# Performance work log

Hardware: AMD Instinct MI355X
Metric: run time of the kernel (lower is better)

## Reference

```python
import jax, jax.numpy as jnp
import numpy as np

B, S, D, N = 8, 4096, 1024, 64
EPS = 1e-5


def setup_inputs() -> dict:
    key = jax.random.key(0)
    ks = jax.random.split(key, 6)
    sD = 1.0 / np.sqrt(D)
    sN = 1.0 / np.sqrt(N)
    return {
        "x": jax.random.normal(ks[0], (B, S, D), dtype=jnp.float32),
        "ln_w": jnp.ones((D,), jnp.float32),
        "ln_b": jnp.zeros((D,), jnp.float32),
        "Wi": jax.random.normal(ks[1], (N, D), jnp.float32) * sD,
        "bi": jnp.zeros((N,), jnp.float32),
        "Wf": jax.random.normal(ks[2], (N, D), jnp.float32) * sD,
        "bf": jnp.zeros((N,), jnp.float32),
        "Wz": jax.random.normal(ks[3], (N, D), jnp.float32) * sD,
        "bz": jnp.zeros((N,), jnp.float32),
        "Wo": jax.random.normal(ks[4], (N, D), jnp.float32) * sD,
        "bo": jnp.zeros((N,), jnp.float32),
        "Wp": jax.random.normal(ks[5], (D, N), jnp.float32) * sN,
        "bp": jnp.zeros((D,), jnp.float32),
    }


def reference(x, ln_w, ln_b, Wi, bi, Wf, bf, Wz, bz, Wo, bo, Wp, bp):
    # LayerNorm over last dim (eps matches torch default 1e-5)
    mu = jnp.mean(x, axis=-1, keepdims=True)
    var = jnp.mean(jnp.square(x - mu), axis=-1, keepdims=True)
    xn = (x - mu) * jax.lax.rsqrt(var + EPS) * ln_w + ln_b

    # Precompute all four projections as batched GEMMs: (B,S,N)
    log_i = jnp.clip(jnp.einsum('bsd,nd->bsn', xn, Wi) + bi, -20.0, 20.0)
    log_f = jnp.clip(jnp.einsum('bsd,nd->bsn', xn, Wf) + bf, -20.0, 20.0)
    z = jnp.tanh(jnp.einsum('bsd,nd->bsn', xn, Wz) + bz)
    o = jax.nn.sigmoid(jnp.einsum('bsd,nd->bsn', xn, Wo) + bo)

    # Stabilized exponential-gated recurrence via lax.scan over time
    def step(carry, inp):
        c, m = carry
        li, lf, zt, ot = inp
        m_new = jnp.maximum(m + lf, li)
        i_s = jnp.exp(li - m_new)
        f_s = jnp.exp(m + lf - m_new)
        c = f_s * c + i_s * zt
        h = ot * jnp.tanh(c)
        return (c, m_new), h

    c0 = jnp.zeros((x.shape[0], log_i.shape[-1]), x.dtype)
    m0 = jnp.zeros_like(c0)
    # time-major inputs: (S,B,N)
    tm = lambda a: jnp.swapaxes(a, 0, 1)
    _, h_seq = jax.lax.scan(step, (c0, m0), (tm(log_i), tm(log_f), tm(z), tm(o)))
    h_seq = jnp.swapaxes(h_seq, 0, 1)  # (B,S,N)

    return jnp.einsum('bsn,dn->bsd', h_seq, Wp) + bp
```

## Files before the change

### kernel.cpp

```cpp
#include <hip/hip_runtime.h>
#include <hip/hip_bf16.h>

#define BB 8
#define SS 4096
#define DD 1024
#define NN 64
#define ROWS (BB * SS)
#define GLD 256
#define NCHUNK 256
#define CLEN 16
#define GSTRIDE 194

typedef _Float16 f16;
using f16x8 = __attribute__((ext_vector_type(8))) _Float16;
using f32x4 = __attribute__((ext_vector_type(4))) float;

__global__ __launch_bounds__(256) void prep_all(const float* __restrict__ Wi, const float* __restrict__ bi,
                                                const float* __restrict__ Wf, const float* __restrict__ bfv,
                                                const float* __restrict__ Wz, const float* __restrict__ bz,
                                                const float* __restrict__ Wo, const float* __restrict__ bo,
                                                const float* __restrict__ Wp,
                                                const float* __restrict__ ln_w, const float* __restrict__ ln_b,
                                                f16* __restrict__ Wpk, f16* __restrict__ Wpf,
                                                float* __restrict__ ball, float* __restrict__ e_all) {
    if (blockIdx.x < 384) {
        int i = blockIdx.x * 256 + threadIdx.x;
        if (i < 32768) {
            int l = i & 63, cb = (i >> 6) & 15, s = i >> 10;
            int r = cb * 16 + (l & 15);
            int c = s * 32 + (l >> 4) * 8;
            int g = r >> 6, rem = r & 63;
            const float* W = (g == 0) ? Wi : (g == 1) ? Wf : (g == 2) ? Wz : Wo;
            const float* src = W + rem * 1024 + c;
            const float* lwp = ln_w + c;
            f16x8 v;
            #pragma unroll
            for (int e = 0; e < 8; ++e) v[e] = (f16)(src[e] * lwp[e]);
            *reinterpret_cast<f16x8*>(Wpk + (size_t)s * 8192 + cb * 512 + l * 8) = v;
        } else if (i < 32768 + 65536) {
            int j = i - 32768;
            Wpf[j] = (f16)Wp[j];
        }
    } else {
        int j = (blockIdx.x - 384) * 4 + (threadIdx.x >> 6);
        int lane = threadIdx.x & 63;
        int g = j >> 6, rem = j & 63;
        const float* W  = (g == 0) ? Wi : (g == 1) ? Wf : (g == 2) ? Wz : Wo;
        const float* bs = (g == 0) ? bi : (g == 1) ? bfv : (g == 2) ? bz : bo;
        const float* row = W + rem * 1024;
        float d = 0.0f, e = 0.0f;
        #pragma unroll
        for (int t = 0; t < 16; ++t) {
            int k = lane + 64 * t;
            float w = row[k];
            e += ln_w[k] * w;
            d += ln_b[k] * w;
        }
        #pragma unroll
        for (int off = 1; off < 64; off <<= 1) {
            e += __shfl_xor(e, off);
            d += __shfl_xor(d, off);
        }
        if (lane == 0) { ball[j] = bs[rem] + d; e_all[j] = e; }
    }
}

__global__ __launch_bounds__(512, 1) void gate_gemm(const float* __restrict__ x,
                                                    const f16* __restrict__ Wpk,
                                                    const float* __restrict__ ball,
                                                    const float* __restrict__ e_all,
                                                    float* __restrict__ gates,
                                                    float4* __restrict__ s4) {
    int bm = blockIdx.x * 128;
    int tid = threadIdx.x;
    int wid = tid >> 6, lane = tid & 63;
    int wm = wid >> 2, wn = wid & 3;
    int lrow = lane & 15, lkg = lane >> 4;
    int srow = tid >> 2, skg = tid & 3;

    __shared__ __align__(16) f16 Wlds[2][16384];
    __shared__ __align__(16) f16 Xlds[2][8192];
    __shared__ float2 stats_lds[128];

    const float4* xrow = reinterpret_cast<const float4*>(x + (size_t)(bm + srow) * DD) + skg * 4;
    float4 A0, A1, A2, A3, B0, B1, B2, B3;
    uint4 W0, W1, W2, W3;
    const uint4* wsrc = reinterpret_cast<const uint4*>(Wpk) + wid * 256 + lane;

    auto loadA = [&](int s) { const float4* p = xrow + s * 16; A0 = p[0]; A1 = p[1]; A2 = p[2]; A3 = p[3]; };
    auto loadB = [&](int s) { const float4* p = xrow + s * 16; B0 = p[0]; B1 = p[1]; B2 = p[2]; B3 = p[3]; };
    auto loadW = [&](int s) { const uint4* p = wsrc + (size_t)s * 2048; W0 = p[0]; W1 = p[64]; W2 = p[128]; W3 = p[192]; };
    auto writeW = [&](int buf) {
        uint4* d = reinterpret_cast<uint4*>((char*)&Wlds[buf][0] + wid * 4096) + lane;
        d[0] = W0; d[64] = W1; d[128] = W2; d[192] = W3;
    };

    float s1 = 0.0f, s2 = 0.0f;
    auto writeXv = [&](float4 v0, float4 v1, float4 v2, float4 v3, int buf) {
        float xv[16] = {v0.x, v0.y, v0.z, v0.w, v1.x, v1.y, v1.z, v1.w,
                        v2.x, v2.y, v2.z, v2.w, v3.x, v3.y, v3.z, v3.w};
        f16x8 p0, p1;
        #pragma unroll
        for (int e = 0; e < 8; ++e) {
            s1 += xv[e] + xv[8 + e];
            s2 += xv[e] * xv[e] + xv[8 + e] * xv[8 + e];
            p0[e] = (f16)xv[e];
            p1[e] = (f16)xv[8 + e];
        }
        char* base = (char*)&Xlds[buf][0] + srow * 128;
        int r7 = srow & 7;
        *reinterpret_cast<f16x8*>(base + 16 * ((2 * skg) ^ r7))     = p0;
        *reinterpret_cast<f16x8*>(base + 16 * ((2 * skg + 1) ^ r7)) = p1;
    };

    f32x4 acc[4][4] = {};
    auto compute = [&](int buf) {
        #pragma unroll
        for (int h = 0; h < 2; ++h) {
            f16x8 a[4];
            #pragma unroll
            for (int mf = 0; mf < 4; ++mf) {
                int row = wm * 64 + mf * 16 + lrow;
                a[mf] = *reinterpret_cast<const f16x8*>(
                    (const char*)&Xlds[buf][0] + row * 128 + 16 * ((4 * h + lkg) ^ (row & 7)));
            }
            #pragma unroll
            for (int nf = 0; nf < 4; ++nf) {
                int cb = wn * 4 + nf;
                f16x8 w = *reinterpret_cast<const f16x8*>(
                    (const char*)&Wlds[buf][0] + h * 16384 + cb * 1024 + lane * 16);
                #pragma unroll
                for (int mf = 0; mf < 4; ++mf)
                    acc[mf][nf] = __builtin_amdgcn_mfma_f32_16x16x32_f16(a[mf], w, acc[mf][nf], 0, 0, 0);
            }
        }
    };
    auto stepSync = [&]() {
        asm volatile("s_waitcnt lgkmcnt(0)" ::: "memory");
        __builtin_amdgcn_s_barrier();
        __builtin_amdgcn_sched_barrier(0);
    };

    loadA(0); loadB(1); loadW(0);
    writeW(0);
    writeXv(A0, A1, A2, A3, 0);
    loadA(2); loadW(1);
    stepSync();

    for (int it = 0; it < 8; ++it) {
        int s = 2 * it;
        compute(0);
        writeW(1);
        writeXv(B0, B1, B2, B3, 1);
        if (s + 2 <= 15) loadW(s + 2);
        if (s + 3 <= 15) loadB(s + 3);
        stepSync();
        compute(1);
        if (s + 2 <= 15) {
            writeW(0);
            writeXv(A0, A1, A2, A3, 0);
        }
        if (s + 3 <= 15) loadW(s + 3);
        if (s + 4 <= 15) loadA(s + 4);
        stepSync();
    }

    s1 += __shfl_xor(s1, 1); s2 += __shfl_xor(s2, 1);
    s1 += __shfl_xor(s1, 2); s2 += __shfl_xor(s2, 2);
    if ((tid & 3) == 0) {
        float mu = s1 * (1.0f / DD);
        float var = s2 * (1.0f / DD) - mu * mu;
        float rsd = rsqrtf(var + 1e-5f);
        float2 st; st.x = mu * rsd; st.y = rsd;
        stats_lds[srow] = st;
    }
    __syncthreads();

    float* glds = reinterpret_cast<float*>(&Wlds[0][0]);
    int c0 = wn * 64;
    int rb = (lane >> 4) * 4;
    #pragma unroll
    for (int mf = 0; mf < 4; ++mf) {
        #pragma unroll
        for (int nf = 0; nf < 4; ++nf) {
            int col = c0 + nf * 16 + (lane & 15);
            float bc = ball[col];
            float ec = e_all[col];
            #pragma unroll
            for (int r = 0; r < 4; ++r) {
                int rl = wm * 64 + mf * 16 + rb + r;
                float2 st = stats_lds[rl];
                float v = acc[mf][nf][r] * st.y + bc - st.x * ec;
                float res;
                if (wn == 0 || wn == 1)      res = fminf(fmaxf(v, -20.0f), 20.0f);
                else if (wn == 2)            res = tanhf(v);
                else                         res = 1.0f / (1.0f + expf(-v));
                gates[(size_t)(bm + rl) * GLD + col] = res;
                if (wm == 0 && wn < 3)
                    glds[(mf * 16 + rb + r) * GSTRIDE + col] = res;
            }
        }
    }
    __syncthreads();

    int b = bm >> 12;
    int cb0 = (bm & 4095) >> 4;
    auto scanChunk = [&]() {
        int lr0 = (wid & 3) * 16;
        float Lf = 0.0f, m = -1e30f, c = 0.0f;
        #pragma unroll
        for (int j = 0; j < 16; ++j) {
            const float* g = glds + (lr0 + j) * GSTRIDE;
            float li = g[lane], lf = g[64 + lane], z = g[128 + lane];
            Lf += lf;
            float ma = m + lf;
            float mn = fmaxf(ma, li);
            c = __expf(ma - mn) * c + __expf(li - mn) * z;
            m = mn;
        }
        float4 v; v.x = Lf; v.y = m; v.z = c; v.w = 0.0f;
        s4[(size_t)(b * NCHUNK + cb0 + wid) * 64 + lane] = v;
    };

    if (wm == 0) scanChunk();
    __syncthreads();

    if (wm == 1 && wn < 3) {
        #pragma unroll
        for (int mf = 0; mf < 4; ++mf) {
            #pragma unroll
            for (int nf = 0; nf < 4; ++nf) {
                int col = c0 + nf * 16 + (lane & 15);
                float bc = ball[col];
                float ec = e_all[col];
                #pragma unroll
                for (int r = 0; r < 4; ++r) {
                    int rl = 64 + mf * 16 + rb + r;
                    float2 st = stats_lds[rl];
                    float v = acc[mf][nf][r] * st.y + bc - st.x * ec;
                    float res;
                    if (wn == 0 || wn == 1)      res = fminf(fmaxf(v, -20.0f), 20.0f);
                    else                         res = tanhf(v);
                    glds[(mf * 16 + rb + r) * GSTRIDE + col] = res;
                }
            }
        }
    }
    __syncthreads();
    if (wm == 1) scanChunk();
}

__global__ __launch_bounds__(64) void scan_b(const float4* __restrict__ s4,
                                             float2* __restrict__ c2) {
    int b = blockIdx.x;
    int n = threadIdx.x;
    size_t base = (size_t)b * NCHUNK * 64 + n;
    float c = 0.0f, m = 0.0f;
    float4 cur[16];
    #pragma unroll
    for (int d = 0; d < 16; ++d) cur[d] = s4[base + (size_t)d * 64];
    for (int kb = 0; kb < NCHUNK; kb += 16) {
        float4 nxt[16];
        if (kb + 16 < NCHUNK) {
            #pragma unroll
            for (int d = 0; d < 16; ++d) nxt[d] = s4[base + (size_t)(kb + 16 + d) * 64];
        }
        #pragma unroll
        for (int d = 0; d < 16; ++d) {
            float2 ci; ci.x = m; ci.y = c;
            c2[base + (size_t)(kb + d) * 64] = ci;
            float4 v = cur[d];
            float ma = m + v.x;
            float mo = fmaxf(ma, v.y);
            c = expf(ma - mo) * c + expf(v.y - mo) * v.z;
            m = mo;
        }
        #pragma unroll
        for (int d = 0; d < 16; ++d) cur[d] = nxt[d];
    }
}

__global__ __launch_bounds__(256) void scan_c(const float* __restrict__ gates,
                                              const float2* __restrict__ c2,
                                              f16* __restrict__ h) {
    int w = blockIdx.x * 4 + (threadIdx.x >> 6);
    int lane = threadIdx.x & 63;
    int b = w >> 8, k = w & (NCHUNK - 1);
    int t0 = k * CLEN;
    float2 ci = c2[(size_t)(b * NCHUNK + k) * 64 + lane];
    float m = ci.x, c = ci.y;
    const float* gp = gates + ((size_t)(b * SS + t0)) * GLD + lane;
    f16* hp = h + ((size_t)(b * SS + t0)) * NN + lane;
    for (int t = 0; t < CLEN; ++t) {
        float li = gp[0], lf = gp[64], z = gp[128], o = gp[192];
        gp += GLD;
        float ma = m + lf;
        float mn = fmaxf(ma, li);
        c = expf(ma - mn) * c + expf(li - mn) * z;
        m = mn;
        *hp = (f16)(o * tanhf(c));
        hp += NN;
    }
}

__global__ __launch_bounds__(256) void out_gemm(const f16* __restrict__ h,
                                                const f16* __restrict__ Wpf,
                                                const float* __restrict__ bp,
                                                float* __restrict__ out) {
    int tid = threadIdx.x, wid = tid >> 6, lane = tid & 63;
    int r0 = (blockIdx.x >> 1) * 32;
    int c0 = (blockIdx.x & 1) * 512 + wid * 128;
    int lrow = lane & 15, lk = (lane >> 4) * 8;

    f32x4 acc[2][8] = {};
    #pragma unroll
    for (int ks = 0; ks < 2; ++ks) {
        int kk = ks * 32;
        f16x8 a[2], bfr[8];
        #pragma unroll
        for (int mf = 0; mf < 2; ++mf)
            a[mf] = *reinterpret_cast<const f16x8*>(h + (size_t)(r0 + mf * 16 + lrow) * NN + kk + lk);
        #pragma unroll
        for (int nf = 0; nf < 8; ++nf)
            bfr[nf] = *reinterpret_cast<const f16x8*>(Wpf + (size_t)(c0 + nf * 16 + lrow) * NN + kk + lk);
        #pragma unroll
        for (int mf = 0; mf < 2; ++mf)
            #pragma unroll
            for (int nf = 0; nf < 8; ++nf)
                acc[mf][nf] = __builtin_amdgcn_mfma_f32_16x16x32_f16(a[mf], bfr[nf], acc[mf][nf], 0, 0, 0);
    }
    int rb = (lane >> 4) * 4;
    #pragma unroll
    for (int nf = 0; nf < 8; ++nf) {
        int col = c0 + nf * 16 + (lane & 15);
        float bias = bp[col];
        #pragma unroll
        for (int mf = 0; mf < 2; ++mf) {
            #pragma unroll
            for (int r = 0; r < 4; ++r) {
                int row = r0 + mf * 16 + rb + r;
                out[(size_t)row * DD + col] = acc[mf][nf][r] + bias;
            }
        }
    }
}

extern "C" void kernel_launch(void* const* d_in, const int* in_sizes, int n_in,
                              void* d_out, int out_size, void* d_ws, size_t ws_size,
                              hipStream_t stream) {
    const float* x    = (const float*)d_in[0];
    const float* ln_w = (const float*)d_in[1];
    const float* ln_b = (const float*)d_in[2];
    const float* Wi   = (const float*)d_in[3];
    const float* bi   = (const float*)d_in[4];
    const float* Wf   = (const float*)d_in[5];
    const float* bfv  = (const float*)d_in[6];
    const float* Wz   = (const float*)d_in[7];
    const float* bz   = (const float*)d_in[8];
    const float* Wo   = (const float*)d_in[9];
    const float* bo   = (const float*)d_in[10];
    const float* Wp   = (const float*)d_in[11];
    const float* bp   = (const float*)d_in[12];
    float* out = (float*)d_out;

    float* gates = (float*)d_out;
    float4* s4 = (float4*)((float*)d_out + 9 * 1024 * 1024);
    float2* c2 = (float2*)((float*)d_out + 10 * 1024 * 1024);

    char* w = (char*)d_ws;
    f16* h    = (f16*)w; w += (size_t)ROWS * NN * 2;
    f16* Wpk  = (f16*)w; w += 32 * 8192 * 2;
    f16* Wpf  = (f16*)w; w += 1024 * 64 * 2;
    float* ball   = (float*)w;    w += 256 * 4;
    float* e_all  = (float*)w;    w += 256 * 4;

    prep_all<<<448, 256, 0, stream>>>(Wi, bi, Wf, bfv, Wz, bz, Wo, bo, Wp,
                                      ln_w, ln_b, Wpk, Wpf, ball, e_all);
    gate_gemm<<<ROWS / 128, 512, 0, stream>>>(x, Wpk, ball, e_all, gates, s4);
    scan_b<<<BB, 64, 0, stream>>>(s4, c2);
    scan_c<<<(BB * NCHUNK) / 4, 256, 0, stream>>>(gates, c2, h);
    out_gemm<<<(ROWS / 32) * 2, 256, 0, stream>>>(h, Wpf, bp, out);
}
```

Baseline: 135.9 us.

## Fuse chunk rescan into output GEMM and single-pass gate chunk scan

Merges the per-chunk recurrence replay (scan_c) into the output projection kernel, so h is built in swizzled LDS instead of being written to and re-read from global memory. Each output block now covers all 1024 columns for 32 rows, which drops one kernel launch and the h round trip. The gate GEMM grows its LDS to 96KB so all 128 rows of gates fit at once, and all 8 waves scan their chunks in one pass instead of two sequential phases. Intermediates move from the output buffer to the workspace. The trade-off is that only 2 of 4 waves do the serial scan while the other two idle, there are more accumulators per wave, and the larger LDS footprint may reduce occupancy.

```diff
diff --git a/kernel.cpp b/kernel.cpp
--- a/kernel.cpp
+++ b/kernel.cpp
@@ -9,7 +9,6 @@
 #define GLD 256
 #define NCHUNK 256
 #define CLEN 16
-#define GSTRIDE 194
 
 typedef _Float16 f16;
 using f16x8 = __attribute__((ext_vector_type(8))) _Float16;
@@ -78,8 +77,7 @@
     int lrow = lane & 15, lkg = lane >> 4;
     int srow = tid >> 2, skg = tid & 3;
 
-    __shared__ __align__(16) f16 Wlds[2][16384];
-    __shared__ __align__(16) f16 Xlds[2][8192];
+    __shared__ __align__(16) char ldsbuf[98304];
     __shared__ float2 stats_lds[128];
 
     const float4* xrow = reinterpret_cast<const float4*>(x + (size_t)(bm + srow) * DD) + skg * 4;
@@ -91,7 +89,7 @@
     auto loadB = [&](int s) { const float4* p = xrow + s * 16; B0 = p[0]; B1 = p[1]; B2 = p[2]; B3 = p[3]; };
     auto loadW = [&](int s) { const uint4* p = wsrc + (size_t)s * 2048; W0 = p[0]; W1 = p[64]; W2 = p[128]; W3 = p[192]; };
     auto writeW = [&](int buf) {
-        uint4* d = reinterpret_cast<uint4*>((char*)&Wlds[buf][0] + wid * 4096) + lane;
+        uint4* d = reinterpret_cast<uint4*>(ldsbuf + buf * 32768 + wid * 4096) + lane;
         d[0] = W0; d[64] = W1; d[128] = W2; d[192] = W3;
     };
 
@@ -107,7 +105,7 @@
             p0[e] = (f16)xv[e];
             p1[e] = (f16)xv[8 + e];
         }
-        char* base = (char*)&Xlds[buf][0] + srow * 128;
+        char* base = ldsbuf + 65536 + buf * 16384 + srow * 128;
         int r7 = srow & 7;
         *reinterpret_cast<f16x8*>(base + 16 * ((2 * skg) ^ r7))     = p0;
         *reinterpret_cast<f16x8*>(base + 16 * ((2 * skg + 1) ^ r7)) = p1;
@@ -122,13 +120,13 @@
             for (int mf = 0; mf < 4; ++mf) {
                 int row = wm * 64 + mf * 16 + lrow;
                 a[mf] = *reinterpret_cast<const f16x8*>(
-                    (const char*)&Xlds[buf][0] + row * 128 + 16 * ((4 * h + lkg) ^ (row & 7)));
+                    ldsbuf + 65536 + buf * 16384 + row * 128 + 16 * ((4 * h + lkg) ^ (row & 7)));
             }
             #pragma unroll
             for (int nf = 0; nf < 4; ++nf) {
                 int cb = wn * 4 + nf;
                 f16x8 w = *reinterpret_cast<const f16x8*>(
-                    (const char*)&Wlds[buf][0] + h * 16384 + cb * 1024 + lane * 16);
+                    ldsbuf + buf * 32768 + h * 16384 + cb * 1024 + lane * 16);
                 #pragma unroll
                 for (int mf = 0; mf < 4; ++mf)
                     acc[mf][nf] = __builtin_amdgcn_mfma_f32_16x16x32_f16(a[mf], w, acc[mf][nf], 0, 0, 0);
@@ -176,7 +174,7 @@
     }
     __syncthreads();
 
-    float* glds = reinterpret_cast<float*>(&Wlds[0][0]);
+    float* glds = reinterpret_cast<float*>(ldsbuf);
     int c0 = wn * 64;
     int rb = (lane >> 4) * 4;
     #pragma unroll
@@ -196,8 +194,8 @@
                 else if (wn == 2)            res = tanhf(v);
                 else                         res = 1.0f / (1.0f + expf(-v));
                 gates[(size_t)(bm + rl) * GLD + col] = res;
-                if (wm == 0 && wn < 3)
-                    glds[(mf * 16 + rb + r) * GSTRIDE + col] = res;
+                if (wn < 3)
+                    glds[rl * 192 + col] = res;
             }
         }
     }
@@ -205,12 +203,12 @@
 
     int b = bm >> 12;
     int cb0 = (bm & 4095) >> 4;
-    auto scanChunk = [&]() {
-        int lr0 = (wid & 3) * 16;
+    {
+        int lr0 = wid * 16;
         float Lf = 0.0f, m = -1e30f, c = 0.0f;
         #pragma unroll
         for (int j = 0; j < 16; ++j) {
-            const float* g = glds + (lr0 + j) * GSTRIDE;
+            const float* g = glds + (lr0 + j) * 192;
             float li = g[lane], lf = g[64 + lane], z = g[128 + lane];
             Lf += lf;
             float ma = m + lf;
@@ -220,34 +218,7 @@
         }
         float4 v; v.x = Lf; v.y = m; v.z = c; v.w = 0.0f;
         s4[(size_t)(b * NCHUNK + cb0 + wid) * 64 + lane] = v;
-    };
-
-    if (wm == 0) scanChunk();
-    __syncthreads();
-
-    if (wm == 1 && wn < 3) {
-        #pragma unroll
-        for (int mf = 0; mf < 4; ++mf) {
-            #pragma unroll
-            for (int nf = 0; nf < 4; ++nf) {
-                int col = c0 + nf * 16 + (lane & 15);
-                float bc = ball[col];
-                float ec = e_all[col];
-                #pragma unroll
-                for (int r = 0; r < 4; ++r) {
-                    int rl = 64 + mf * 16 + rb + r;
-                    float2 st = stats_lds[rl];
-                    float v = acc[mf][nf][r] * st.y + bc - st.x * ec;
-                    float res;
-                    if (wn == 0 || wn == 1)      res = fminf(fmaxf(v, -20.0f), 20.0f);
-                    else                         res = tanhf(v);
-                    glds[(mf * 16 + rb + r) * GSTRIDE + col] = res;
-                }
-            }
-        }
-    }
-    __syncthreads();
-    if (wm == 1) scanChunk();
+    }
 }
 
 __global__ __launch_bounds__(64) void scan_b(const float4* __restrict__ s4,
@@ -280,59 +251,62 @@
     }
 }
 
-__global__ __launch_bounds__(256) void scan_c(const float* __restrict__ gates,
-                                              const float2* __restrict__ c2,
-                                              f16* __restrict__ h) {
-    int w = blockIdx.x * 4 + (threadIdx.x >> 6);
-    int lane = threadIdx.x & 63;
-    int b = w >> 8, k = w & (NCHUNK - 1);
-    int t0 = k * CLEN;
-    float2 ci = c2[(size_t)(b * NCHUNK + k) * 64 + lane];
-    float m = ci.x, c = ci.y;
-    const float* gp = gates + ((size_t)(b * SS + t0)) * GLD + lane;
-    f16* hp = h + ((size_t)(b * SS + t0)) * NN + lane;
-    for (int t = 0; t < CLEN; ++t) {
-        float li = gp[0], lf = gp[64], z = gp[128], o = gp[192];
-        gp += GLD;
-        float ma = m + lf;
-        float mn = fmaxf(ma, li);
-        c = expf(ma - mn) * c + expf(li - mn) * z;
-        m = mn;
-        *hp = (f16)(o * tanhf(c));
-        hp += NN;
-    }
-}
-
-__global__ __launch_bounds__(256) void out_gemm(const f16* __restrict__ h,
-                                                const f16* __restrict__ Wpf,
-                                                const float* __restrict__ bp,
-                                                float* __restrict__ out) {
+__global__ __launch_bounds__(256) void out_fused(const float* __restrict__ gates,
+                                                 const float2* __restrict__ c2,
+                                                 const f16* __restrict__ Wpf,
+                                                 const float* __restrict__ bp,
+                                                 float* __restrict__ out) {
     int tid = threadIdx.x, wid = tid >> 6, lane = tid & 63;
-    int r0 = (blockIdx.x >> 1) * 32;
-    int c0 = (blockIdx.x & 1) * 512 + wid * 128;
-    int lrow = lane & 15, lk = (lane >> 4) * 8;
-
-    f32x4 acc[2][8] = {};
+    int r0 = blockIdx.x * 32;
+    int b = r0 >> 12;
+    int k0 = (r0 & 4095) >> 4;
+
+    __shared__ __align__(16) f16 hlds[32 * 64];
+
+    if (wid < 2) {
+        int k = k0 + wid;
+        float2 ci = c2[((size_t)b * NCHUNK + k) * 64 + lane];
+        float m = ci.x, c = ci.y;
+        const float* gp = gates + (size_t)(r0 + wid * 16) * GLD + lane;
+        #pragma unroll
+        for (int t = 0; t < 16; ++t) {
+            float li = gp[0], lf = gp[64], z = gp[128], o = gp[192];
+            gp += GLD;
+            float ma = m + lf;
+            float mn = fmaxf(ma, li);
+            c = __expf(ma - mn) * c + __expf(li - mn) * z;
+            m = mn;
+            int row = wid * 16 + t;
+            hlds[row * 64 + (((lane >> 3) ^ (row & 7)) << 3) + (lane & 7)] = (f16)(o * tanhf(c));
+        }
+    }
+    __syncthreads();
+
+    int c0 = wid * 256;
+    int lrow = lane & 15, lkg = lane >> 4;
+    f32x4 acc[2][16] = {};
     #pragma unroll
     for (int ks = 0; ks < 2; ++ks) {
         int kk = ks * 32;
-        f16x8 a[2], bfr[8];
-        #pragma unroll
-        for (int mf = 0; mf < 2; ++mf)
-            a[mf] = *reinterpret_cast<const f16x8*>(h + (size_t)(r0 + mf * 16 + lrow) * NN + kk + lk);
-        #pragma unroll
-        for (int nf = 0; nf < 8; ++nf)
-            bfr[nf] = *reinterpret_cast<const f16x8*>(Wpf + (size_t)(c0 + nf * 16 + lrow) * NN + kk + lk);
-        #pragma unroll
-        for (int mf = 0; mf < 2; ++mf)
-            #pragma unroll
-            for (int nf = 0; nf < 8; ++nf)
-                acc[mf][nf] = __builtin_amdgcn_mfma_f32_16x16x32_f16(a[mf], bfr[nf], acc[mf][nf], 0, 0, 0);
-    }
-    int rb = (lane >> 4) * 4;
+        f16x8 a[2];
+        #pragma unroll
+        for (int mf = 0; mf < 2; ++mf) {
+            int row = mf * 16 + lrow;
+            int slot = (kk >> 3) + lkg;
+            a[mf] = *reinterpret_cast<const f16x8*>(&hlds[row * 64 + ((slot ^ (row & 7)) << 3)]);
+        }
+        #pragma unroll
+        for (int nf = 0; nf < 16; ++nf) {
+            f16x8 bfr = *reinterpret_cast<const f16x8*>(Wpf + (size_t)(c0 + nf * 16 + lrow) * NN + kk + lkg * 8);
+            #pragma unroll
+            for (int mf = 0; mf < 2; ++mf)
+                acc[mf][nf] = __builtin_amdgcn_mfma_f32_16x16x32_f16(a[mf], bfr, acc[mf][nf], 0, 0, 0);
+        }
+    }
+    int rb = lkg * 4;
     #pragma unroll
-    for (int nf = 0; nf < 8; ++nf) {
-        int col = c0 + nf * 16 + (lane & 15);
+    for (int nf = 0; nf < 16; ++nf) {
+        int col = c0 + nf * 16 + lrow;
         float bias = bp[col];
         #pragma unroll
         for (int mf = 0; mf < 2; ++mf) {
@@ -363,21 +337,18 @@
     const float* bp   = (const float*)d_in[12];
     float* out = (float*)d_out;
 
-    float* gates = (float*)d_out;
-    float4* s4 = (float4*)((float*)d_out + 9 * 1024 * 1024);
-    float2* c2 = (float2*)((float*)d_out + 10 * 1024 * 1024);
-
     char* w = (char*)d_ws;
-    f16* h    = (f16*)w; w += (size_t)ROWS * NN * 2;
-    f16* Wpk  = (f16*)w; w += 32 * 8192 * 2;
-    f16* Wpf  = (f16*)w; w += 1024 * 64 * 2;
-    float* ball   = (float*)w;    w += 256 * 4;
-    float* e_all  = (float*)w;    w += 256 * 4;
+    float* gates = (float*)w;  w += (size_t)ROWS * GLD * 4;
+    float4* s4   = (float4*)w; w += (size_t)BB * NCHUNK * 64 * 16;
+    float2* c2   = (float2*)w; w += (size_t)BB * NCHUNK * 64 * 8;
+    f16* Wpk     = (f16*)w;    w += 32 * 8192 * 2;
+    f16* Wpf     = (f16*)w;    w += 1024 * 64 * 2;
+    float* ball  = (float*)w;  w += 256 * 4;
+    float* e_all = (float*)w;  w += 256 * 4;
 
     prep_all<<<448, 256, 0, stream>>>(Wi, bi, Wf, bfv, Wz, bz, Wo, bo, Wp,
                                       ln_w, ln_b, Wpk, Wpf, ball, e_all);
     gate_gemm<<<ROWS / 128, 512, 0, stream>>>(x, Wpk, ball, e_all, gates, s4);
     scan_b<<<BB, 64, 0, stream>>>(s4, c2);
-    scan_c<<<(BB * NCHUNK) / 4, 256, 0, stream>>>(gates, c2, h);
-    out_gemm<<<(ROWS / 32) * 2, 256, 0, stream>>>(h, Wpf, bp, out);
-}
+    out_fused<<<ROWS / 32, 256, 0, stream>>>(gates, c2, Wpf, bp, out);
+}
```

After: 136.5 us. No clear change (+0.4%).
